# Performance work log

Measured on AMD Instinct MI355X. Metric: run time of the kernel, lower is better.

## Reference

```python
import jax, jax.numpy as jnp
import numpy as np

P = 2048
IMG_H = IMG_W = 128
FOV = 1.0471975512  # 60 deg vertical/horizontal fov
ZNEAR, ZFAR = 0.01, 100.0
SH_C0 = 0.28209479177387814
LOWPASS = 0.3  # 3DGS low-pass filter added to 2D covariance diagonal


def _camera():
    view = np.eye(4, dtype=np.float32)
    view[2, 3] = 4.0  # camera at world z=-4 looking down +z
    tanf = np.tan(FOV / 2)
    pm = np.zeros((4, 4), dtype=np.float32)
    pm[0, 0] = 1.0 / tanf
    pm[1, 1] = 1.0 / tanf
    pm[2, 2] = ZFAR / (ZFAR - ZNEAR)
    pm[2, 3] = -ZFAR * ZNEAR / (ZFAR - ZNEAR)
    pm[3, 2] = 1.0
    proj = (pm @ view).astype(np.float32)
    campos = np.array([0.0, 0.0, -4.0], dtype=np.float32)
    return view, proj, campos


def setup_inputs() -> dict:
    key = jax.random.key(0)
    ks = jax.random.split(key, 6)
    view, proj, campos = _camera()
    return {
        'means_3d': jax.random.normal(ks[0], (P, 3), dtype=jnp.float32) * 0.8,
        'means_2d': jnp.zeros((P, 2), dtype=jnp.float32),
        'features': jax.random.uniform(ks[1], (P, 3), dtype=jnp.float32),
        'opacities': jax.random.uniform(ks[2], (P, 1), dtype=jnp.float32) * 0.9 + 0.05,
        'scales': jax.random.uniform(ks[3], (P, 3), dtype=jnp.float32) * 0.08 + 0.01,
        'rotations': jax.random.normal(ks[4], (P, 4), dtype=jnp.float32),
        'viewmatrix': jnp.asarray(view),
        'projmatrix': jnp.asarray(proj),
        'campos': jnp.asarray(campos),
        'image_height': IMG_H,
        'image_width': IMG_W,
    }


def _quat_to_rot(q):
    q = q / jnp.linalg.norm(q, axis=-1, keepdims=True)
    w, x, y, z = q[:, 0], q[:, 1], q[:, 2], q[:, 3]
    R = jnp.stack([
        1 - 2 * (y * y + z * z), 2 * (x * y - w * z), 2 * (x * z + w * y),
        2 * (x * y + w * z), 1 - 2 * (x * x + z * z), 2 * (y * z - w * x),
        2 * (x * z - w * y), 2 * (y * z + w * x), 1 - 2 * (x * x + y * y),
    ], axis=-1).reshape(-1, 3, 3)
    return R


def _rasterize(means_3d, features, opacities, scales, rotations, viewmatrix, projmatrix, H, W):
    tanf = jnp.tan(FOV / 2)
    focal_x = W / (2.0 * tanf)
    focal_y = H / (2.0 * tanf)

    # camera-space positions [P,3]
    t = means_3d @ viewmatrix[:3, :3].T + viewmatrix[:3, 3]
    depth = t[:, 2]

    # projected pixel centers (ndc2pix)
    ph = means_3d @ projmatrix[:3, :3].T + projmatrix[:3, 3]
    pw = means_3d @ projmatrix[3, :3] + projmatrix[3, 3]
    ndc = ph[:, :2] / (pw[:, None] + 1e-7)
    px = ((ndc[:, 0] + 1.0) * W - 1.0) * 0.5
    py = ((ndc[:, 1] + 1.0) * H - 1.0) * 0.5

    # 3D covariance: Sigma = R S S^T R^T
    Rm = _quat_to_rot(rotations)
    M = Rm * scales[:, None, :]  # R @ diag(s)
    sigma = M @ jnp.swapaxes(M, 1, 2)  # [P,3,3]

    # EWA splat: 2D covariance = J W Sigma W^T J^T
    lim = 1.3 * tanf
    tz = depth
    tx = jnp.clip(t[:, 0] / tz, -lim, lim) * tz
    ty = jnp.clip(t[:, 1] / tz, -lim, lim) * tz
    zeros = jnp.zeros_like(tz)
    J = jnp.stack([
        jnp.stack([focal_x / tz, zeros, -focal_x * tx / (tz * tz)], -1),
        jnp.stack([zeros, focal_y / tz, -focal_y * ty / (tz * tz)], -1),
    ], axis=1)  # [P,2,3]
    Tm = J @ viewmatrix[:3, :3]
    cov2d = Tm @ sigma @ jnp.swapaxes(Tm, 1, 2)  # [P,2,2]
    a = cov2d[:, 0, 0] + LOWPASS
    b = cov2d[:, 0, 1]
    c = cov2d[:, 1, 1] + LOWPASS
    det = a * c - b * b
    valid = (depth > 0.2) & (det > 0.0)
    det_s = jnp.where(valid, det, 1.0)
    conic_a, conic_b, conic_c = c / det_s, -b / det_s, a / det_s

    # radii from max eigenvalue
    mid = 0.5 * (a + c)
    lam = mid + jnp.sqrt(jnp.maximum(mid * mid - det, 0.1))
    radii = jnp.where(valid, jnp.ceil(3.0 * jnp.sqrt(lam)), 0.0)

    # SH degree-0 color
    color = jnp.maximum(SH_C0 * features + 0.5, 0.0)  # [P,3]

    # depth sort, front to back
    order = jnp.argsort(jnp.where(valid, depth, jnp.inf))
    px_s, py_s = px[order], py[order]
    ca, cb, cc = conic_a[order], conic_b[order], conic_c[order]
    op_s = opacities[order, 0]
    col_s = color[order]
    valid_s = valid[order]

    # pixel grid
    gx, gy = jnp.meshgrid(jnp.arange(W, dtype=jnp.float32), jnp.arange(H, dtype=jnp.float32))
    gx = gx.reshape(-1)
    gy = gy.reshape(-1)  # [HW]

    dx = gx[None, :] - px_s[:, None]  # [P,HW]
    dy = gy[None, :] - py_s[:, None]
    power = -0.5 * (ca[:, None] * dx * dx + cc[:, None] * dy * dy) - cb[:, None] * dx * dy
    alpha = jnp.minimum(0.99, op_s[:, None] * jnp.exp(jnp.minimum(power, 0.0)))
    skip = (power > 0.0) | (alpha < 1.0 / 255.0) | (~valid_s)[:, None]
    alpha = jnp.where(skip, 0.0, alpha)

    one_m = 1.0 - alpha
    incl = jnp.cumprod(one_m, axis=0)
    T_excl = jnp.concatenate([jnp.ones((1, H * W), dtype=alpha.dtype), incl[:-1]], axis=0)
    w = T_excl * alpha  # [P,HW]
    img = jnp.einsum('pn,pc->cn', w, col_s)  # [3,HW]
    T_final = incl[-1]
    img = img + T_final[None, :]  # bg_color = (1,1,1)
    return img.reshape(3, H, W), radii


def reference(means_3d, means_2d, features, opacities, scales, rotations, viewmatrix, projmatrix, campos, image_height, image_width):
    # means_2d and campos are interface placeholders (means_2d receives grads only
    # inside the CUDA kernel; campos only matters for sh_degree > 0)
    return _rasterize(means_3d, features, opacities, scales, rotations, viewmatrix, projmatrix, image_height, image_width)
```

## Files before the change

### kernel.cpp

```cpp
#include <hip/hip_runtime.h>
#include <math.h>


#define IMG 128
#define NPIX (IMG * IMG)
#define GS 12
#define SORT_N 2048
#define KCH 16
#define CHUNK (SORT_N / KCH)

__device__ __forceinline__ void gproj(int i,
                                      const float* __restrict__ means,
                                      const float* __restrict__ rots,
                                      const float* __restrict__ scales,
                                      const float* __restrict__ vm,
                                      const float* __restrict__ pm,
                                      float& depth, bool& valid,
                                      float& px, float& py,
                                      float& ca, float& cb, float& cc,
                                      float& lam)
{
    const float W = (float)IMG, H = (float)IMG;
    const float tanfov = 0.5773502691896258f;
    const float focal_x = W / (2.0f * tanfov);
    const float focal_y = H / (2.0f * tanfov);
    const float lim = 1.3f * tanfov;

    float mx = means[3 * i + 0], my = means[3 * i + 1], mz = means[3 * i + 2];

    float tx = vm[0] * mx + vm[1] * my + vm[2]  * mz + vm[3];
    float ty = vm[4] * mx + vm[5] * my + vm[6]  * mz + vm[7];
    float tz = vm[8] * mx + vm[9] * my + vm[10] * mz + vm[11];
    depth = tz;

    float ph0 = pm[0]  * mx + pm[1]  * my + pm[2]  * mz + pm[3];
    float ph1 = pm[4]  * mx + pm[5]  * my + pm[6]  * mz + pm[7];
    float pw  = pm[12] * mx + pm[13] * my + pm[14] * mz + pm[15];
    float rinv = 1.0f / (pw + 1e-7f);
    px = ((ph0 * rinv + 1.0f) * W - 1.0f) * 0.5f;
    py = ((ph1 * rinv + 1.0f) * H - 1.0f) * 0.5f;

    float qw = rots[4 * i + 0], qx = rots[4 * i + 1], qy = rots[4 * i + 2], qz = rots[4 * i + 3];
    float qn = sqrtf(qw * qw + qx * qx + qy * qy + qz * qz);
    qw /= qn; qx /= qn; qy /= qn; qz /= qn;
    float R00 = 1.0f - 2.0f * (qy * qy + qz * qz), R01 = 2.0f * (qx * qy - qw * qz), R02 = 2.0f * (qx * qz + qw * qy);
    float R10 = 2.0f * (qx * qy + qw * qz), R11 = 1.0f - 2.0f * (qx * qx + qz * qz), R12 = 2.0f * (qy * qz - qw * qx);
    float R20 = 2.0f * (qx * qz - qw * qy), R21 = 2.0f * (qy * qz + qw * qx), R22 = 1.0f - 2.0f * (qx * qx + qy * qy);

    float sx = scales[3 * i + 0], sy = scales[3 * i + 1], sz = scales[3 * i + 2];
    float M00 = R00 * sx, M01 = R01 * sy, M02 = R02 * sz;
    float M10 = R10 * sx, M11 = R11 * sy, M12 = R12 * sz;
    float M20 = R20 * sx, M21 = R21 * sy, M22 = R22 * sz;
    float S00 = M00 * M00 + M01 * M01 + M02 * M02;
    float S01 = M00 * M10 + M01 * M11 + M02 * M12;
    float S02 = M00 * M20 + M01 * M21 + M02 * M22;
    float S11 = M10 * M10 + M11 * M11 + M12 * M12;
    float S12 = M10 * M20 + M11 * M21 + M12 * M22;
    float S22 = M20 * M20 + M21 * M21 + M22 * M22;

    float txc = fminf(fmaxf(tx / tz, -lim), lim) * tz;
    float tyc = fminf(fmaxf(ty / tz, -lim), lim) * tz;
    float J00 = focal_x / tz, J02 = -focal_x * txc / (tz * tz);
    float J11 = focal_y / tz, J12 = -focal_y * tyc / (tz * tz);

    float T00 = J00 * vm[0] + J02 * vm[8];
    float T01 = J00 * vm[1] + J02 * vm[9];
    float T02 = J00 * vm[2] + J02 * vm[10];
    float T10 = J11 * vm[4] + J12 * vm[8];
    float T11 = J11 * vm[5] + J12 * vm[9];
    float T12 = J11 * vm[6] + J12 * vm[10];

    float U00 = T00 * S00 + T01 * S01 + T02 * S02;
    float U01 = T00 * S01 + T01 * S11 + T02 * S12;
    float U02 = T00 * S02 + T01 * S12 + T02 * S22;
    float U10 = T10 * S00 + T11 * S01 + T12 * S02;
    float U11 = T10 * S01 + T11 * S11 + T12 * S12;
    float U12 = T10 * S02 + T11 * S12 + T12 * S22;
    float C00 = U00 * T00 + U01 * T01 + U02 * T02;
    float C01 = U00 * T10 + U01 * T11 + U02 * T12;
    float C11 = U10 * T10 + U11 * T11 + U12 * T12;

    float a = C00 + 0.3f, b = C01, c = C11 + 0.3f;
    float det = a * c - b * b;
    valid = (depth > 0.2f) && (det > 0.0f);
    float det_s = valid ? det : 1.0f;
    ca = c / det_s; cb = -b / det_s; cc = a / det_s;

    float mid = 0.5f * (a + c);
    lam = mid + sqrtf(fmaxf(mid * mid - det, 0.1f));
}

__global__ void gsplat_prep_rank_scatter(const float* __restrict__ means,
                                         const float* __restrict__ feats,
                                         const float* __restrict__ ops,
                                         const float* __restrict__ scales,
                                         const float* __restrict__ rots,
                                         const float* __restrict__ vm,
                                         const float* __restrict__ pm,
                                         float* __restrict__ gS,
                                         float4* __restrict__ culls,
                                         float* __restrict__ radii_out,
                                         int P)
{
    __shared__ unsigned int sk[SORT_N];
    __shared__ int partial[256];
    int tid = threadIdx.x;

    #pragma unroll 2
    for (int j = tid; j < SORT_N; j += 256) {
        unsigned int key = 0xFFFFFFFFu;
        if (j < P) {
            float mx = means[3 * j + 0], my = means[3 * j + 1], mz = means[3 * j + 2];
            float tz = vm[8] * mx + vm[9] * my + vm[10] * mz + vm[11];
            key = (tz > 0.2f) ? __float_as_uint(tz) : 0x7f800000u;
        }
        sk[j] = key;
    }
    __syncthreads();

    int g = tid & 63, s = tid >> 6;
    int i = blockIdx.x * 64 + g;
    bool act = (i < P);
    unsigned int ki = act ? sk[i] : 0u;

    const int SLICE = SORT_N / 4;
    int j0 = s * SLICE;
    const uint4* sk4 = (const uint4*)(sk + j0);
    int r = 0;
    #pragma unroll 4
    for (int q = 0; q < SLICE / 4; ++q) {
        uint4 k = sk4[q];
        int j = j0 + 4 * q;
        r += (k.x < ki) || (k.x == ki && (j + 0) < i);
        r += (k.y < ki) || (k.y == ki && (j + 1) < i);
        r += (k.z < ki) || (k.z == ki && (j + 2) < i);
        r += (k.w < ki) || (k.w == ki && (j + 3) < i);
    }
    partial[tid] = r;
    __syncthreads();

    if (s == 0 && act) {
        int rank = partial[g] + partial[64 + g] + partial[128 + g] + partial[192 + g];

        float depth, px, py, ca, cb, cc, lam; bool valid;
        gproj(i, means, rots, scales, vm, pm, depth, valid, px, py, ca, cb, cc, lam);

        const float SH_C0 = 0.28209479177387814f;
        float colr = fmaxf(SH_C0 * feats[3 * i + 0] + 0.5f, 0.0f);
        float colg = fmaxf(SH_C0 * feats[3 * i + 1] + 0.5f, 0.0f);
        float colb = fmaxf(SH_C0 * feats[3 * i + 2] + 0.5f, 0.0f);

        float opv = ops[i];
        float r2;
        if (valid) {
            r2 = 2.0f * lam * __logf(255.0f * opv) * 1.02f + 0.5f;
        } else {
            px = 0.0f; py = 0.0f; ca = 0.0f; cb = 0.0f; cc = 0.0f;
            opv = 0.0f; r2 = -1.0f;
        }
        radii_out[i] = valid ? ceilf(3.0f * sqrtf(lam)) : 0.0f;

        float4* dst = (float4*)(gS + (size_t)rank * GS);
        dst[0] = make_float4(px, py, ca, cb);
        dst[1] = make_float4(cc, opv, colr, colg);
        dst[2] = make_float4(colb, r2, 0.0f, 0.0f);
        culls[rank] = make_float4(px, py, r2, 0.0f);
    }
}

__global__ void __launch_bounds__(256, 4)
gsplat_raster_chunk(const float* __restrict__ gS,
                    const float4* __restrict__ culls,
                    int P, float4* __restrict__ part)
{
    int tid = threadIdx.x;
    int lx = tid & 15, ly = tid >> 4;
    int lane = tid & 63;
    int tilex = blockIdx.x & 7, tiley = blockIdx.x >> 3;
    int x = tilex * 16 + lx, y = tiley * 16 + ly;
    float gx = (float)x, gy = (float)y;
    float tx0 = (float)(tilex * 16), tx1 = (float)(tilex * 16 + 15);
    float ty0 = (float)(tiley * 16), ty1 = (float)(tiley * 16 + 15);

    int base = blockIdx.y * CHUNK;
    int cnt = min(CHUNK, P - base);

    float T = 1.0f, cr = 0.0f, cg = 0.0f, cb = 0.0f;
    const float* Gp = gS + (size_t)base * GS;

    float4 cu0 = culls[base + lane];
    float4 cu1 = culls[base + 64 + lane];

    #pragma unroll
    for (int half = 0; half < 2; ++half) {
        int h = half * 64;
        float4 cu = (half == 0) ? cu0 : cu1;
        bool pred = false;
        if (h + lane < cnt) {
            float ddx = cu.x - fminf(fmaxf(cu.x, tx0), tx1);
            float ddy = cu.y - fminf(fmaxf(cu.y, ty0), ty1);
            pred = (ddx * ddx + ddy * ddy <= cu.z);
        }
        unsigned long long m = __ballot(pred);
        while (m) {
            int b0 = __builtin_ctzll(m); m &= m - 1;
            int n = 1, b1 = b0, b2 = b0, b3 = b0;
            if (m) { b1 = __builtin_ctzll(m); m &= m - 1; n = 2;
                if (m) { b2 = __builtin_ctzll(m); m &= m - 1; n = 3;
                    if (m) { b3 = __builtin_ctzll(m); m &= m - 1; n = 4; } } }

            const float4* R0 = (const float4*)(Gp + (size_t)(h + b0) * GS);
            const float4* R1 = (const float4*)(Gp + (size_t)(h + b1) * GS);
            const float4* R2 = (const float4*)(Gp + (size_t)(h + b2) * GS);
            const float4* R3 = (const float4*)(Gp + (size_t)(h + b3) * GS);
            float4 A0 = R0[0], B0 = R0[1], C0 = R0[2];
            float4 A1 = R1[0], B1 = R1[1], C1 = R1[2];
            float4 A2 = R2[0], B2 = R2[1], C2 = R2[2];
            float4 A3 = R3[0], B3 = R3[1], C3 = R3[2];

            float dx0 = gx - A0.x, dy0 = gy - A0.y;
            float p0 = -0.5f * (A0.z * dx0 * dx0 + B0.x * dy0 * dy0) - A0.w * dx0 * dy0;
            float a0 = fminf(0.99f, B0.y * __expf(fminf(p0, 0.0f)));
            a0 = (p0 > 0.0f) ? 0.0f : a0;
            a0 = (a0 < 0.00392156862745098f) ? 0.0f : a0;

            float dx1 = gx - A1.x, dy1 = gy - A1.y;
            float p1 = -0.5f * (A1.z * dx1 * dx1 + B1.x * dy1 * dy1) - A1.w * dx1 * dy1;
            float a1 = fminf(0.99f, B1.y * __expf(fminf(p1, 0.0f)));
            a1 = (p1 > 0.0f) ? 0.0f : a1;
            a1 = (a1 < 0.00392156862745098f) ? 0.0f : a1;

            float dx2 = gx - A2.x, dy2 = gy - A2.y;
            float p2 = -0.5f * (A2.z * dx2 * dx2 + B2.x * dy2 * dy2) - A2.w * dx2 * dy2;
            float a2 = fminf(0.99f, B2.y * __expf(fminf(p2, 0.0f)));
            a2 = (p2 > 0.0f) ? 0.0f : a2;
            a2 = (a2 < 0.00392156862745098f) ? 0.0f : a2;

            float dx3 = gx - A3.x, dy3 = gy - A3.y;
            float p3 = -0.5f * (A3.z * dx3 * dx3 + B3.x * dy3 * dy3) - A3.w * dx3 * dy3;
            float a3 = fminf(0.99f, B3.y * __expf(fminf(p3, 0.0f)));
            a3 = (p3 > 0.0f) ? 0.0f : a3;
            a3 = (a3 < 0.00392156862745098f) ? 0.0f : a3;

            float w;
            w = T * a0; cr = fmaf(w, B0.z, cr); cg = fmaf(w, B0.w, cg); cb = fmaf(w, C0.x, cb); T *= (1.0f - a0);
            if (n > 1) { w = T * a1; cr = fmaf(w, B1.z, cr); cg = fmaf(w, B1.w, cg); cb = fmaf(w, C1.x, cb); T *= (1.0f - a1); }
            if (n > 2) { w = T * a2; cr = fmaf(w, B2.z, cr); cg = fmaf(w, B2.w, cg); cb = fmaf(w, C2.x, cb); T *= (1.0f - a2); }
            if (n > 3) { w = T * a3; cr = fmaf(w, B3.z, cr); cg = fmaf(w, B3.w, cg); cb = fmaf(w, C3.x, cb); T *= (1.0f - a3); }
        }
    }

    int pix = y * IMG + x;
    part[(size_t)blockIdx.y * NPIX + pix] = make_float4(cr, cg, cb, T);
}

__global__ void gsplat_combine(const float4* __restrict__ part,
                               float* __restrict__ img)
{
    int pix = blockIdx.x * blockDim.x + threadIdx.x;
    if (pix >= NPIX) return;
    float4 v[KCH];
    #pragma unroll
    for (int c = 0; c < KCH; ++c)
        v[c] = part[(size_t)c * NPIX + pix];
    float T = 1.0f, r = 0.0f, g = 0.0f, b = 0.0f;
    #pragma unroll
    for (int c = 0; c < KCH; ++c) {
        r = fmaf(T, v[c].x, r);
        g = fmaf(T, v[c].y, g);
        b = fmaf(T, v[c].z, b);
        T *= v[c].w;
    }
    img[pix]            = r + T;
    img[NPIX + pix]     = g + T;
    img[2 * NPIX + pix] = b + T;
}

extern "C" void kernel_launch(void* const* d_in, const int* in_sizes, int n_in,
                              void* d_out, int out_size, void* d_ws, size_t ws_size,
                              hipStream_t stream)
{
    const float* means  = (const float*)d_in[0];
    const float* feats  = (const float*)d_in[2];
    const float* ops    = (const float*)d_in[3];
    const float* scales = (const float*)d_in[4];
    const float* rots   = (const float*)d_in[5];
    const float* vm     = (const float*)d_in[6];
    const float* pm     = (const float*)d_in[7];

    int P = in_sizes[0] / 3;

    float* img   = (float*)d_out;
    float* radii = (float*)d_out + 3 * NPIX;

    float*  gS    = (float*)d_ws;
    float4* culls = (float4*)(gS + (size_t)SORT_N * GS);
    float4* part  = culls + SORT_N;

    gsplat_prep_rank_scatter<<<(P + 63) / 64, 256, 0, stream>>>(
        means, feats, ops, scales, rots, vm, pm, gS, culls, radii, P);

    gsplat_raster_chunk<<<dim3(64, KCH), 256, 0, stream>>>(gS, culls, P, part);

    gsplat_combine<<<NPIX / 256, 256, 0, stream>>>(part, img);
}
```

Baseline: 104.2 us.

## Fuse chunk combine into raster via last-block ticket; widen rank kernel to 512

Removes the separate combine kernel launch. Each raster block writes its partial into a tile-local slab, then takes an atomic ticket, and the last chunk block for each tile composites all 16 partials into the image. The prep/rank kernel moves to 512 threads, so the rank count splits into 8 slices instead of 4, and block 0 resets the tickets. This saves one launch and improves locality of the partial buffer, at the cost of threadfence/atomic overhead and a serialized combine tail in the last block per tile.

```diff
diff --git a/kernel.cpp b/kernel.cpp
--- a/kernel.cpp
+++ b/kernel.cpp
@@ -8,6 +8,7 @@
 #define SORT_N 2048
 #define KCH 16
 #define CHUNK (SORT_N / KCH)
+#define NTILE 64
 
 __device__ __forceinline__ void gproj(int i,
                                       const float* __restrict__ means,
@@ -90,24 +91,28 @@
     lam = mid + sqrtf(fmaxf(mid * mid - det, 0.1f));
 }
 
-__global__ void gsplat_prep_rank_scatter(const float* __restrict__ means,
-                                         const float* __restrict__ feats,
-                                         const float* __restrict__ ops,
-                                         const float* __restrict__ scales,
-                                         const float* __restrict__ rots,
-                                         const float* __restrict__ vm,
-                                         const float* __restrict__ pm,
-                                         float* __restrict__ gS,
-                                         float4* __restrict__ culls,
-                                         float* __restrict__ radii_out,
-                                         int P)
+__global__ void __launch_bounds__(512)
+gsplat_prep_rank_scatter(const float* __restrict__ means,
+                         const float* __restrict__ feats,
+                         const float* __restrict__ ops,
+                         const float* __restrict__ scales,
+                         const float* __restrict__ rots,
+                         const float* __restrict__ vm,
+                         const float* __restrict__ pm,
+                         float* __restrict__ gS,
+                         float4* __restrict__ culls,
+                         float* __restrict__ radii_out,
+                         unsigned int* __restrict__ tickets,
+                         int P)
 {
     __shared__ unsigned int sk[SORT_N];
-    __shared__ int partial[256];
+    __shared__ int partial[512];
     int tid = threadIdx.x;
 
+    if (blockIdx.x == 0 && tid < NTILE) tickets[tid] = 0u;
+
     #pragma unroll 2
-    for (int j = tid; j < SORT_N; j += 256) {
+    for (int j = tid; j < SORT_N; j += 512) {
         unsigned int key = 0xFFFFFFFFu;
         if (j < P) {
             float mx = means[3 * j + 0], my = means[3 * j + 1], mz = means[3 * j + 2];
@@ -123,7 +128,7 @@
     bool act = (i < P);
     unsigned int ki = act ? sk[i] : 0u;
 
-    const int SLICE = SORT_N / 4;
+    const int SLICE = SORT_N / 8;
     int j0 = s * SLICE;
     const uint4* sk4 = (const uint4*)(sk + j0);
     int r = 0;
@@ -140,7 +145,9 @@
     __syncthreads();
 
     if (s == 0 && act) {
-        int rank = partial[g] + partial[64 + g] + partial[128 + g] + partial[192 + g];
+        int rank = 0;
+        #pragma unroll
+        for (int k = 0; k < 8; ++k) rank += partial[64 * k + g];
 
         float depth, px, py, ca, cb, cc, lam; bool valid;
         gproj(i, means, rots, scales, vm, pm, depth, valid, px, py, ca, cb, cc, lam);
@@ -169,20 +176,24 @@
 }
 
 __global__ void __launch_bounds__(256, 4)
-gsplat_raster_chunk(const float* __restrict__ gS,
+gsplat_raster_fused(const float* __restrict__ gS,
                     const float4* __restrict__ culls,
-                    int P, float4* __restrict__ part)
+                    int P, float4* __restrict__ part,
+                    unsigned int* __restrict__ tickets,
+                    float* __restrict__ img)
 {
     int tid = threadIdx.x;
     int lx = tid & 15, ly = tid >> 4;
     int lane = tid & 63;
-    int tilex = blockIdx.x & 7, tiley = blockIdx.x >> 3;
+    int tile = blockIdx.x;
+    int kc = blockIdx.y;
+    int tilex = tile & 7, tiley = tile >> 3;
     int x = tilex * 16 + lx, y = tiley * 16 + ly;
     float gx = (float)x, gy = (float)y;
     float tx0 = (float)(tilex * 16), tx1 = (float)(tilex * 16 + 15);
     float ty0 = (float)(tiley * 16), ty1 = (float)(tiley * 16 + 15);
 
-    int base = blockIdx.y * CHUNK;
+    int base = kc * CHUNK;
     int cnt = min(CHUNK, P - base);
 
     float T = 1.0f, cr = 0.0f, cg = 0.0f, cb = 0.0f;
@@ -250,30 +261,41 @@
         }
     }
 
-    int pix = y * IMG + x;
-    part[(size_t)blockIdx.y * NPIX + pix] = make_float4(cr, cg, cb, T);
-}
-
-__global__ void gsplat_combine(const float4* __restrict__ part,
-                               float* __restrict__ img)
-{
-    int pix = blockIdx.x * blockDim.x + threadIdx.x;
-    if (pix >= NPIX) return;
-    float4 v[KCH];
-    #pragma unroll
-    for (int c = 0; c < KCH; ++c)
-        v[c] = part[(size_t)c * NPIX + pix];
-    float T = 1.0f, r = 0.0f, g = 0.0f, b = 0.0f;
-    #pragma unroll
-    for (int c = 0; c < KCH; ++c) {
-        r = fmaf(T, v[c].x, r);
-        g = fmaf(T, v[c].y, g);
-        b = fmaf(T, v[c].z, b);
-        T *= v[c].w;
-    }
-    img[pix]            = r + T;
-    img[NPIX + pix]     = g + T;
-    img[2 * NPIX + pix] = b + T;
+    float4* slab = part + ((size_t)tile * KCH) * 256;
+    slab[kc * 256 + tid] = make_float4(cr, cg, cb, T);
+    __threadfence();
+    __syncthreads();
+    __shared__ unsigned int s_old;
+    if (tid == 0) s_old = atomicAdd(&tickets[tile], 1u);
+    __syncthreads();
+
+    if (s_old == KCH - 1) {
+        __threadfence();
+        float4 v[8];
+        float Tt = 1.0f, r = 0.0f, g = 0.0f, b = 0.0f;
+        #pragma unroll
+        for (int c = 0; c < 8; ++c) v[c] = slab[c * 256 + tid];
+        #pragma unroll
+        for (int c = 0; c < 8; ++c) {
+            r = fmaf(Tt, v[c].x, r);
+            g = fmaf(Tt, v[c].y, g);
+            b = fmaf(Tt, v[c].z, b);
+            Tt *= v[c].w;
+        }
+        #pragma unroll
+        for (int c = 0; c < 8; ++c) v[c] = slab[(8 + c) * 256 + tid];
+        #pragma unroll
+        for (int c = 0; c < 8; ++c) {
+            r = fmaf(Tt, v[c].x, r);
+            g = fmaf(Tt, v[c].y, g);
+            b = fmaf(Tt, v[c].z, b);
+            Tt *= v[c].w;
+        }
+        int pix = y * IMG + x;
+        img[pix]            = r + Tt;
+        img[NPIX + pix]     = g + Tt;
+        img[2 * NPIX + pix] = b + Tt;
+    }
 }
 
 extern "C" void kernel_launch(void* const* d_in, const int* in_sizes, int n_in,
@@ -293,14 +315,14 @@
     float* img   = (float*)d_out;
     float* radii = (float*)d_out + 3 * NPIX;
 
-    float*  gS    = (float*)d_ws;
-    float4* culls = (float4*)(gS + (size_t)SORT_N * GS);
-    float4* part  = culls + SORT_N;
-
-    gsplat_prep_rank_scatter<<<(P + 63) / 64, 256, 0, stream>>>(
-        means, feats, ops, scales, rots, vm, pm, gS, culls, radii, P);
-
-    gsplat_raster_chunk<<<dim3(64, KCH), 256, 0, stream>>>(gS, culls, P, part);
-
-    gsplat_combine<<<NPIX / 256, 256, 0, stream>>>(part, img);
+    float*        gS      = (float*)d_ws;
+    float4*       culls   = (float4*)(gS + (size_t)SORT_N * GS);
+    float4*       part    = culls + SORT_N;
+    unsigned int* tickets = (unsigned int*)(part + (size_t)NTILE * KCH * 256);
+
+    gsplat_prep_rank_scatter<<<(P + 63) / 64, 512, 0, stream>>>(
+        means, feats, ops, scales, rots, vm, pm, gS, culls, radii, tickets, P);
+
+    gsplat_raster_fused<<<dim3(NTILE, KCH), 256, 0, stream>>>(
+        gS, culls, P, part, tickets, img);
 }
```

After: 173.1 us. 1.66x slower.
